# Kernel tuning notes

Hardware: AMD Instinct MI355X
Metric: run time of the kernel (lower is better)

## Reference

```python
import jax, jax.numpy as jnp
import numpy as np

NPG = 400          # nodes per graph (CC400 atlas ROIs)
B = 512            # graphs per batch
N = B * NPG        # total nodes
EPG = 6400         # edges per graph (avg degree 16)
E = B * EPG
F_IN = 200         # node feature dim
H = 64             # hidden_channels
C = 2              # num_classes


def _lin(k, fi, fo):
    return jax.random.normal(k, (fi, fo), jnp.float32) / np.sqrt(fi)


def setup_inputs() -> dict:
    key = jax.random.key(0)
    ks = jax.random.split(key, 16)
    # intra-graph edges: local src/dst in [0, NPG) plus per-graph offset
    g = jnp.repeat(jnp.arange(B, dtype=jnp.int32), EPG)
    src = jax.random.randint(ks[0], (E,), 0, NPG, dtype=jnp.int32) + g * NPG
    dst = jax.random.randint(ks[1], (E,), 0, NPG, dtype=jnp.int32) + g * NPG
    edge_index = jnp.stack([src, dst])  # [2, E]
    x = jax.random.normal(ks[2], (N, F_IN), jnp.float32)
    return dict(
        x=x, edge_index=edge_index, npg=NPG,
        # SAGEConv i: out = lin_l(mean_agg) + lin_r(x); lin_l carries the bias
        W1l=_lin(ks[3], F_IN, H), W1r=_lin(ks[4], F_IN, H), b1=jnp.zeros((H,), jnp.float32),
        W2l=_lin(ks[5], H, H), W2r=_lin(ks[6], H, H), b2=jnp.zeros((H,), jnp.float32),
        W3l=_lin(ks[7], H, H), W3r=_lin(ks[8], H, H), b3=jnp.zeros((H,), jnp.float32),
        # SAGPooling score GNN = GraphConv(H, 1): lin_rel(sum_agg) + lin_root(x)
        Wpr=_lin(ks[9], H, 1), bpr=jnp.zeros((1,), jnp.float32), Wpo=_lin(ks[10], H, 1),
        # final classifier
        Wlin=_lin(ks[11], H, C), blin=jnp.zeros((C,), jnp.float32),
    )


def reference(x, edge_index, npg, W1l, W1r, b1, W2l, W2r, b2, W3l, W3r, b3,
              Wpr, bpr, Wpo, Wlin, blin):
    n = x.shape[0]
    src, dst = edge_index[0], edge_index[1]

    deg = jax.ops.segment_sum(jnp.ones((src.shape[0],), x.dtype), dst, num_segments=n)
    inv_deg = 1.0 / jnp.maximum(deg, 1.0)  # [n]

    def sage(h, Wl, Wr, b):
        # mean aggregation over incoming edges, then lin_l(agg)+b + lin_r(h)
        agg = jax.ops.segment_sum(h[src], dst, num_segments=n) * inv_deg[:, None]
        return agg @ Wl + b + h @ Wr

    x1 = jax.nn.relu(sage(x, W1l, W1r, b1))
    x2 = jax.nn.relu(sage(x1, W2l, W2r, b2)) + x1
    x3 = jax.nn.relu(sage(x2, W3l, W3r, b3)) + x2

    # SAGPooling score via GraphConv (add aggregation)
    score = (jax.ops.segment_sum(x3[src], dst, num_segments=n) @ Wpr + bpr
             + x3 @ Wpo)[:, 0]  # [n]

    nb = n // npg            # number of graphs
    k = npg // 2             # ratio = 0.5, uniform graph sizes
    vals, idx = jax.lax.top_k(score.reshape(nb, npg), k)       # [nb, k]
    flat_idx = (jnp.arange(nb, dtype=idx.dtype)[:, None] * npg + idx).reshape(-1)
    xp = x3[flat_idx] * jnp.tanh(vals.reshape(-1))[:, None]    # [nb*k, H]

    pooled = xp.reshape(nb, k, -1).mean(axis=1)                # global_mean_pool
    logits = pooled @ Wlin + blin
    return jax.nn.log_softmax(logits, axis=1)
```

## Files before the change

kernel.cpp:

```cpp
#include <hip/hip_runtime.h>
#include <hip/hip_bf16.h>
#include <math.h>

#define F_IN 200
#define HDIM 64
#define NPG  400
#define EPG  6400
#define KSEL 200

typedef __attribute__((ext_vector_type(4))) float f32x4;
typedef __attribute__((ext_vector_type(8))) short s16x8;

__device__ __forceinline__ void gload_lds16(const void* g, void* l) {
    __builtin_amdgcn_global_load_lds(
        (const __attribute__((address_space(1))) void*)g,
        (__attribute__((address_space(3))) void*)l, 16, 0, 0);
}

__device__ __forceinline__ unsigned int bf16_rne(float x) {
    unsigned int b = __float_as_uint(x);
    return (b + 0x7FFFu + ((b >> 16) & 1u)) >> 16;
}

__device__ __forceinline__ void split8(f32x4 v0, f32x4 v1, s16x8& h, s16x8& l) {
    float x[8] = {v0.x, v0.y, v0.z, v0.w, v1.x, v1.y, v1.z, v1.w};
#pragma unroll
    for (int j = 0; j < 8; j++) {
        unsigned int hb = bf16_rne(x[j]);
        float hf = __uint_as_float(hb << 16);
        float r = x[j] - hf;
        unsigned int lb = bf16_rne(r);
        h[j] = (short)hb;
        l[j] = (short)lb;
    }
}

__global__ void pack_wf(const float* __restrict__ Wl, const float* __restrict__ Wr,
                        short* __restrict__ WF, int K, int KC) {
    int idx = blockIdx.x * blockDim.x + threadIdx.x;
    if (idx >= KC * 4096) return;
    int j    = idx & 7;
    int lane = (idx >> 3) & 63;
    int nf   = (idx >> 9) & 7;
    int kc   = idx >> 12;
    int k = kc * 32 + (lane >> 4) * 8 + j;
    int n = nf * 16 + (lane & 15);
    float v = 0.f;
    if (k < K) v = (n < 64) ? Wl[k * 64 + n] : Wr[k * 64 + (n - 64)];
    unsigned int hb = bf16_rne(v);
    float hf = __uint_as_float(hb << 16);
    unsigned int lb = bf16_rne(v - hf);
    WF[(size_t)((kc * 8 + nf) * 2 + 0) * 512 + lane * 8 + j] = (short)hb;
    WF[(size_t)((kc * 8 + nf) * 2 + 1) * 512 + lane * 8 + j] = (short)lb;
}

__global__ void pack_wf4(const float* __restrict__ Wl, const float* __restrict__ Wr,
                         short* __restrict__ WF) {
    int idx = blockIdx.x * blockDim.x + threadIdx.x;
    if (idx >= 4 * 2048) return;
    int j    = idx & 7;
    int lane = (idx >> 3) & 63;
    int nf   = (idx >> 9) & 3;
    int kc   = idx >> 11;
    int k = kc * 32 + (lane >> 4) * 8 + j;
    int n = nf * 16 + (lane & 15);
    float v = (k < 64) ? Wl[k * 64 + n] : Wr[(k - 64) * 64 + n];
    unsigned int hb = bf16_rne(v);
    float hf = __uint_as_float(hb << 16);
    unsigned int lb = bf16_rne(v - hf);
    WF[(size_t)((kc * 4 + nf) * 2 + 0) * 512 + lane * 8 + j] = (short)hb;
    WF[(size_t)((kc * 4 + nf) * 2 + 1) * 512 + lane * 8 + j] = (short)lb;
}

template <int K, int LDX, int KC, int TAIL>
__global__ __launch_bounds__(256) void gemm_lds(const float* __restrict__ X,
                                                const short* __restrict__ WF,
                                                float* __restrict__ O) {
    __shared__ float Xs[2][128 * 32];
    __shared__ short Ws[2][8 * 2 * 512];
    const int tid  = threadIdx.x;
    const int lane = tid & 63;
    const int wave = tid >> 6;
    const size_t rowbase = (size_t)blockIdx.x * 128;
    const f32x4 zero4 = (f32x4){0.f, 0.f, 0.f, 0.f};

    const int srow_off = wave * 32 + (lane >> 3);
    const int sbyte    = 16 * ((lane & 7) ^ (lane >> 3));

#define DMA_CHUNK(b, kc_) {                                                      \
    _Pragma("unroll")                                                            \
    for (int j = 0; j < 4; j++) {                                                \
        const char* xsrc = (const char*)X +                                      \
            (rowbase + srow_off + j * 8) * (size_t)(LDX * 4) + (kc_) * 128 + sbyte; \
        gload_lds16(xsrc, (char*)&Xs[b][0] + wave * 4096 + j * 1024);            \
        const short* wsrc = WF + (size_t)(kc_) * 8192 + wave * 2048 + j * 512 + lane * 8; \
        gload_lds16(wsrc, (char*)&Ws[b][0] + wave * 4096 + j * 1024);            \
    } }

    f32x4 acc[2][8];
#pragma unroll
    for (int m = 0; m < 2; m++)
#pragma unroll
        for (int nf = 0; nf < 8; nf++) acc[m][nf] = zero4;

    DMA_CHUNK(0, 0);
    __syncthreads();

    for (int kc = 0; kc < KC; kc++) {
        const int b = kc & 1;
        if (kc + 1 < KC) DMA_CHUNK(b ^ 1, kc + 1);

        s16x8 ah[2], al[2];
#pragma unroll
        for (int m = 0; m < 2; m++) {
            const int lr = wave * 32 + m * 16 + (lane & 15);
            const int g0 = (lane >> 4) * 2;
            f32x4 v0 = *(const f32x4*)&Xs[b][lr * 32 + 4 * (g0 ^ (lane & 7))];
            f32x4 v1 = *(const f32x4*)&Xs[b][lr * 32 + 4 * ((g0 + 1) ^ (lane & 7))];
            split8(v0, v1, ah[m], al[m]);
        }
#pragma unroll
        for (int nf = 0; nf < 8; nf++) {
            s16x8 wh = *(const s16x8*)&Ws[b][(nf * 2 + 0) * 512 + lane * 8];
            s16x8 wl = *(const s16x8*)&Ws[b][(nf * 2 + 1) * 512 + lane * 8];
#pragma unroll
            for (int m = 0; m < 2; m++) {
                acc[m][nf] = __builtin_amdgcn_mfma_f32_16x16x32_bf16(ah[m], wh, acc[m][nf], 0, 0, 0);
                acc[m][nf] = __builtin_amdgcn_mfma_f32_16x16x32_bf16(al[m], wh, acc[m][nf], 0, 0, 0);
                acc[m][nf] = __builtin_amdgcn_mfma_f32_16x16x32_bf16(ah[m], wl, acc[m][nf], 0, 0, 0);
            }
        }
        __syncthreads();
    }
#undef DMA_CHUNK

    if constexpr (TAIL > 0) {
        s16x8 ah[2], al[2];
#pragma unroll
        for (int m = 0; m < 2; m++) {
            const size_t row = rowbase + wave * 32 + m * 16 + (lane & 15);
            const int k0 = KC * 32 + (lane >> 4) * 8;
            f32x4 v0 = (k0 + 4 <= K) ? *(const f32x4*)&X[row * (size_t)LDX + k0] : zero4;
            f32x4 v1 = (k0 + 8 <= K) ? *(const f32x4*)&X[row * (size_t)LDX + k0 + 4] : zero4;
            split8(v0, v1, ah[m], al[m]);
        }
#pragma unroll
        for (int nf = 0; nf < 8; nf++) {
            s16x8 wh = *(const s16x8*)&WF[(size_t)((KC * 8 + nf) * 2 + 0) * 512 + lane * 8];
            s16x8 wl = *(const s16x8*)&WF[(size_t)((KC * 8 + nf) * 2 + 1) * 512 + lane * 8];
#pragma unroll
            for (int m = 0; m < 2; m++) {
                acc[m][nf] = __builtin_amdgcn_mfma_f32_16x16x32_bf16(ah[m], wh, acc[m][nf], 0, 0, 0);
                acc[m][nf] = __builtin_amdgcn_mfma_f32_16x16x32_bf16(al[m], wh, acc[m][nf], 0, 0, 0);
                acc[m][nf] = __builtin_amdgcn_mfma_f32_16x16x32_bf16(ah[m], wl, acc[m][nf], 0, 0, 0);
            }
        }
    }

    float* cs0 = &Xs[0][wave * 1024];
    float* cs1 = &Xs[1][wave * 1024];
#pragma unroll
    for (int m = 0; m < 2; m++) {
        const int scol = lane & 15;
        const int srow = (lane >> 4) * 4;
#pragma unroll
        for (int nf = 0; nf < 8; nf++)
#pragma unroll
            for (int r = 0; r < 4; r++) {
                int cr = srow + r;
                float* p = (cr < 8) ? cs0 + cr * 128 : cs1 + (cr - 8) * 128;
                p[nf * 16 + scol] = acc[m][nf][r];
            }
#pragma unroll
        for (int ps = 0; ps < 8; ps++) {
            int row = ps * 2 + (lane >> 5);
            const float* p = (row < 8) ? cs0 + row * 128 : cs1 + (row - 8) * 128;
            f32x4 v = *(const f32x4*)&p[(lane & 31) * 4];
            *(f32x4*)&O[(rowbase + wave * 32 + m * 16 + row) * 128 + (lane & 31) * 4] = v;
        }
    }
}

__global__ __launch_bounds__(256) void combine_ss(
    const float* __restrict__ M, const float* __restrict__ H,
    const short* __restrict__ WF, const float* __restrict__ bias,
    const float* __restrict__ resid, float* __restrict__ P)
{
    __shared__ float Xs[4][64 * 32];
    __shared__ short Ws[4][4096];
    const int tid  = threadIdx.x;
    const int lane = tid & 63;
    const int wave = tid >> 6;
    const size_t rowbase = (size_t)blockIdx.x * 64;

#pragma unroll
    for (int c = 0; c < 4; c++) {
        const float* srcbuf = (c < 2) ? M : H;
#pragma unroll
        for (int i = 0; i < 2; i++) {
            int rr = i * 8 + (lane >> 3);
            int jj = (lane & 7) ^ (rr & 7);
            const char* src = (const char*)(srcbuf + (rowbase + wave * 16 + rr) * 64)
                              + (c & 1) * 128 + jj * 16;
            gload_lds16(src, (char*)&Xs[c][0] + wave * 2048 + i * 1024 + lane * 16);
        }
#pragma unroll
        for (int t = 0; t < 2; t++) {
            int idx = t * 256 + tid;
            const short* wsrc = WF + (size_t)c * 4096 + idx * 8;
            gload_lds16(wsrc, (char*)&Ws[c][0] + idx * 16);
        }
    }
    __syncthreads();

    f32x4 acc[4];
#pragma unroll
    for (int nf = 0; nf < 4; nf++) acc[nf] = (f32x4){0.f, 0.f, 0.f, 0.f};

    const int r = lane & 15;
    const int j0 = (lane >> 4) * 2;
#pragma unroll
    for (int kc = 0; kc < 4; kc++) {
        const float* abase = &Xs[kc][wave * 512 + r * 32];
        f32x4 v0 = *(const f32x4*)&abase[((j0    ) ^ (r & 7)) * 4];
        f32x4 v1 = *(const f32x4*)&abase[((j0 + 1) ^ (r & 7)) * 4];
        s16x8 ah, al;
        split8(v0, v1, ah, al);
#pragma unroll
        for (int nf = 0; nf < 4; nf++) {
            s16x8 wh = *(const s16x8*)&Ws[kc][(nf * 2 + 0) * 512 + lane * 8];
            s16x8 wl = *(const s16x8*)&Ws[kc][(nf * 2 + 1) * 512 + lane * 8];
            acc[nf] = __builtin_amdgcn_mfma_f32_16x16x32_bf16(ah, wh, acc[nf], 0, 0, 0);
            acc[nf] = __builtin_amdgcn_mfma_f32_16x16x32_bf16(al, wh, acc[nf], 0, 0, 0);
            acc[nf] = __builtin_amdgcn_mfma_f32_16x16x32_bf16(ah, wl, acc[nf], 0, 0, 0);
        }
    }

    {
        float* cs0 = &Xs[0][wave * 512];
        float* cs1 = &Xs[1][wave * 512];
        const int scol = lane & 15;
        const int srow = (lane >> 4) * 4;
#pragma unroll
        for (int nf = 0; nf < 4; nf++)
#pragma unroll
            for (int ri = 0; ri < 4; ri++) {
                int cr = srow + ri;
                float* p = (cr < 8) ? cs0 + cr * 64 : cs1 + (cr - 8) * 64;
                p[nf * 16 + scol] = acc[nf][ri];
            }
#pragma unroll
        for (int i = 0; i < 4; i++) {
            int row = i * 4 + (lane >> 4);
            int col = (lane & 15) * 4;
            const float* p = (row < 8) ? cs0 + row * 64 : cs1 + (row - 8) * 64;
            f32x4 v = *(const f32x4*)&p[col];
            size_t grow = rowbase + wave * 16 + row;
            f32x4 bb = *(const f32x4*)&bias[col];
            f32x4 rr = *(const f32x4*)&resid[grow * 64 + col];
            f32x4 o;
#pragma unroll
            for (int q = 0; q < 4; q++) o[q] = fmaxf(v[q] + bb[q], 0.f) + rr[q];
            *(f32x4*)&P[grow * 64 + col] = o;
        }
    }
}

__global__ __launch_bounds__(256) void csr_build(
    const int* __restrict__ esrc, const int* __restrict__ edst,
    int* __restrict__ csr_src, int* __restrict__ rowptr,
    int* __restrict__ degs, float* __restrict__ invdeg)
{
    __shared__ int cnt[NPG];
    __shared__ int off[NPG];
    __shared__ int cur[NPG];
    const int g = blockIdx.x, tid = threadIdx.x;
    const int ebase = g * EPG, nodebase = g * NPG;
    for (int i = tid; i < NPG; i += 256) cnt[i] = 0;
    __syncthreads();
    for (int e = tid; e < EPG; e += 256)
        atomicAdd(&cnt[edst[ebase + e] - nodebase], 1);
    __syncthreads();
    if (tid == 0) {
        int run = 0;
        for (int i = 0; i < NPG; i++) { off[i] = run; run += cnt[i]; }
    }
    __syncthreads();
    for (int i = tid; i < NPG; i += 256) {
        cur[i] = off[i];
        rowptr[nodebase + i] = off[i];
        degs[nodebase + i] = cnt[i];
        invdeg[nodebase + i] = 1.f / fmaxf((float)cnt[i], 1.f);
    }
    __syncthreads();
    for (int e = tid; e < EPG; e += 256) {
        int ld = edst[ebase + e] - nodebase;
        int p = atomicAdd(&cur[ld], 1);
        csr_src[ebase + p] = esrc[ebase + e] - nodebase;
    }
}

__global__ __launch_bounds__(1024) void agg_lds(
    const float* __restrict__ A,
    const int* __restrict__ csr_src, const int* __restrict__ rowptr,
    const int* __restrict__ degs, const float* __restrict__ invdeg,
    const float* __restrict__ bias,
    float* __restrict__ Xout)
{
    __shared__ float y[NPG * 64];
    __shared__ int   csr_l[EPG];
    const int g = blockIdx.x, tid = threadIdx.x;
    const int ebase = g * EPG, nodebase = g * NPG;

    for (int idx = tid; idx < NPG * 16; idx += 1024) {
        int node = idx >> 4, c4 = (idx & 15) * 4;
        *(float4*)&y[node * 64 + c4] =
            *(const float4*)&A[(size_t)(nodebase + node) * 128 + c4];
    }
    for (int e = tid; e < EPG; e += 1024) csr_l[e] = csr_src[ebase + e];
    __syncthreads();

    const int wave = tid >> 6, lane = tid & 63;
    for (int node = wave; node < NPG; node += 16) {
        const int start = rowptr[nodebase + node];
        const int dg = degs[nodebase + node];
        float acc = 0.f;
        int j = 0;
        for (; j + 4 <= dg; j += 4) {
            int s0 = csr_l[start + j];
            int s1 = csr_l[start + j + 1];
            int s2 = csr_l[start + j + 2];
            int s3 = csr_l[start + j + 3];
            acc += y[s0 * 64 + lane] + y[s1 * 64 + lane]
                 + y[s2 * 64 + lane] + y[s3 * 64 + lane];
        }
        for (; j < dg; j++) acc += y[csr_l[start + j] * 64 + lane];

        float v = acc * invdeg[nodebase + node] + bias[lane]
                + A[(size_t)(nodebase + node) * 128 + 64 + lane];
        Xout[(size_t)(nodebase + node) * 64 + lane] = fmaxf(v, 0.f);
    }
}

__global__ __launch_bounds__(1024) void agg_in(
    const float* __restrict__ H,
    const int* __restrict__ csr_src, const int* __restrict__ rowptr,
    const int* __restrict__ degs, const float* __restrict__ invdeg,
    float* __restrict__ M)
{
    __shared__ float y[NPG * 64];
    __shared__ int   csr_l[EPG];
    const int g = blockIdx.x, tid = threadIdx.x;
    const int ebase = g * EPG, nodebase = g * NPG;

    for (int idx = tid; idx < NPG * 16; idx += 1024) {
        int node = idx >> 4, c4 = (idx & 15) * 4;
        *(float4*)&y[node * 64 + c4] =
            *(const float4*)&H[(size_t)(nodebase + node) * 64 + c4];
    }
    for (int e = tid; e < EPG; e += 1024) csr_l[e] = csr_src[ebase + e];
    __syncthreads();

    const int wave = tid >> 6, lane = tid & 63;
    for (int node = wave; node < NPG; node += 16) {
        const int start = rowptr[nodebase + node];
        const int dg = degs[nodebase + node];
        float acc = 0.f;
        int j = 0;
        for (; j + 4 <= dg; j += 4) {
            int s0 = csr_l[start + j];
            int s1 = csr_l[start + j + 1];
            int s2 = csr_l[start + j + 2];
            int s3 = csr_l[start + j + 3];
            acc += y[s0 * 64 + lane] + y[s1 * 64 + lane]
                 + y[s2 * 64 + lane] + y[s3 * 64 + lane];
        }
        for (; j < dg; j++) acc += y[csr_l[start + j] * 64 + lane];

        M[(size_t)(nodebase + node) * 64 + lane] = acc * invdeg[nodebase + node];
    }
}

__global__ __launch_bounds__(1024) void score_pool3(
    const float* __restrict__ X3,
    const int* __restrict__ esrc, const int* __restrict__ edst,
    const float* __restrict__ Wpr, const float* __restrict__ bpr,
    const float* __restrict__ Wpo,
    const float* __restrict__ Wlin, const float* __restrict__ blin,
    float* __restrict__ out)
{
    __shared__ float y[NPG * 64];
    __shared__ float t0s[NPG], ss[NPG], wsel[NPG];
    __shared__ float wprs[64], wpos[64];
    __shared__ float pp[16 * 64];
    __shared__ float pooled[64];
    __shared__ float lgs[2];
    const int g = blockIdx.x, tid = threadIdx.x;
    const int nodebase = g * NPG, ebase = g * EPG;

    if (tid < 64) { wprs[tid] = Wpr[tid]; wpos[tid] = Wpo[tid]; }
    for (int idx = tid; idx < NPG * 16; idx += 1024) {
        int node = idx >> 4, c4 = (idx & 15) * 4;
        *(float4*)&y[node * 64 + c4] =
            *(const float4*)&X3[(size_t)(nodebase + node) * 64 + c4];
    }
    __syncthreads();

    if (tid < NPG) {
        float a0 = 0.f, a1 = 0.f;
        const float* yr = &y[tid * 64];
#pragma unroll
        for (int i = 0; i < 64; i++) {
            int d = (tid + i) & 63;
            float v = yr[d];
            a0 += v * wprs[d];
            a1 += v * wpos[d];
        }
        t0s[tid] = a0;
        ss[tid] = bpr[0] + a1;
    }
    __syncthreads();
    for (int e = tid; e < EPG; e += 1024) {
        int ls = esrc[ebase + e] - nodebase;
        int ld = edst[ebase + e] - nodebase;
        atomicAdd(&ss[ld], t0s[ls]);
    }
    __syncthreads();
    if (tid < NPG) {
        float si = ss[tid];
        int cnt = 0;
        for (int j = 0; j < NPG; j++) {
            float sj = ss[j];
            cnt += (sj > si) || (sj == si && j < tid);
        }
        wsel[tid] = (cnt < KSEL) ? tanhf(si) * (1.f / KSEL) : 0.f;
    }
    __syncthreads();
    {
        const int d = tid & 63, part = tid >> 6;
        float a = 0.f;
        for (int i = part * 25; i < part * 25 + 25; i++)
            a += wsel[i] * y[i * 64 + d];
        pp[part * 64 + d] = a;
    }
    __syncthreads();
    if (tid < 64) {
        float s = 0.f;
#pragma unroll
        for (int i = 0; i < 16; i++) s += pp[i * 64 + tid];
        pooled[tid] = s;
    }
    __syncthreads();
    if (tid < 2) {
        float l = blin[tid];
        for (int d = 0; d < 64; d++) l += pooled[d] * Wlin[d * 2 + tid];
        lgs[tid] = l;
    }
    __syncthreads();
    if (tid < 2) {
        float m = fmaxf(lgs[0], lgs[1]);
        float lse = m + logf(expf(lgs[0] - m) + expf(lgs[1] - m));
        out[g * 2 + tid] = lgs[tid] - lse;
    }
}

extern "C" void kernel_launch(void* const* d_in, const int* in_sizes, int n_in,
                              void* d_out, int out_size, void* d_ws, size_t ws_size,
                              hipStream_t stream) {
    const float* x    = (const float*)d_in[0];
    const int*   eidx = (const int*)d_in[1];
    const float* W1l  = (const float*)d_in[3];
    const float* W1r  = (const float*)d_in[4];
    const float* b1   = (const float*)d_in[5];
    const float* W2l  = (const float*)d_in[6];
    const float* W2r  = (const float*)d_in[7];
    const float* b2   = (const float*)d_in[8];
    const float* W3l  = (const float*)d_in[9];
    const float* W3r  = (const float*)d_in[10];
    const float* b3   = (const float*)d_in[11];
    const float* Wpr  = (const float*)d_in[12];
    const float* bpr  = (const float*)d_in[13];
    const float* Wpo  = (const float*)d_in[14];
    const float* Wlin = (const float*)d_in[15];
    const float* blin = (const float*)d_in[16];

    const int N = in_sizes[0] / F_IN;
    const int E = in_sizes[1] / 2;
    const int B = N / NPG;
    const int* esrc = eidx;
    const int* edst = eidx + E;

    float* ws = (float*)d_ws;
    float* A      = ws;
    float* P0     = A + (size_t)N * 128;
    float* P1     = P0 + (size_t)N * 64;
    float* Mb     = P1 + (size_t)N * 64;
    float* invdeg = Mb + (size_t)N * 64;
    short* WF1    = (short*)(invdeg + N);
    short* WFc2   = WF1 + 57344;
    short* WFc3   = WFc2 + 16384;
    int*   csr    = (int*)(WFc3 + 16384);
    int*   rowptr = csr + E;
    int*   degs   = rowptr + N;

    pack_wf<<<(7 * 4096 + 255) / 256, 256, 0, stream>>>(W1l, W1r, WF1, 200, 7);
    pack_wf4<<<(4 * 2048 + 255) / 256, 256, 0, stream>>>(W2l, W2r, WFc2);
    pack_wf4<<<(4 * 2048 + 255) / 256, 256, 0, stream>>>(W3l, W3r, WFc3);

    csr_build<<<B, 256, 0, stream>>>(esrc, edst, csr, rowptr, degs, invdeg);

    gemm_lds<200, 200, 6, 8><<<N / 128, 256, 0, stream>>>(x, WF1, A);
    agg_lds<<<B, 1024, 0, stream>>>(A, csr, rowptr, degs, invdeg, b1, P0);

    agg_in<<<B, 1024, 0, stream>>>(P0, csr, rowptr, degs, invdeg, Mb);
    combine_ss<<<N / 64, 256, 0, stream>>>(Mb, P0, WFc2, b2, P0, P1);

    agg_in<<<B, 1024, 0, stream>>>(P1, csr, rowptr, degs, invdeg, Mb);
    combine_ss<<<N / 64, 256, 0, stream>>>(Mb, P1, WFc3, b3, P1, P0);

    score_pool3<<<B, 1024, 0, stream>>>(P0, esrc, edst,
                                        Wpr, bpr, Wpo, Wlin, blin,
                                        (float*)d_out);
}
```

Before: 438.2 us.

## Rewrite first-layer GEMM to stage full 64-row X tile in LDS

Replaces the double-buffered 128-row, 32-wide-chunk GEMM with a kernel that loads a whole 64x200 slab of X into padded LDS in one DMA pass. It then loops over K, reading the pre-split bf16 weight fragments straight from global memory (cached) rather than staging them in LDS. Rows per block drop from 128 to 64, which doubles the grid and halves the MFMA work per wave. The aim is fewer barriers and more occupancy and parallelism, at the cost of repeated global weight reads and no overlap between loading and compute.

```diff
diff --git a/kernel.cpp b/kernel.cpp
--- a/kernel.cpp
+++ b/kernel.cpp
@@ -72,111 +72,65 @@
     WF[(size_t)((kc * 4 + nf) * 2 + 1) * 512 + lane * 8 + j] = (short)lb;
 }
 
-template <int K, int LDX, int KC, int TAIL>
-__global__ __launch_bounds__(256) void gemm_lds(const float* __restrict__ X,
-                                                const short* __restrict__ WF,
-                                                float* __restrict__ O) {
-    __shared__ float Xs[2][128 * 32];
-    __shared__ short Ws[2][8 * 2 * 512];
-    const int tid  = threadIdx.x;
-    const int lane = tid & 63;
-    const int wave = tid >> 6;
-    const size_t rowbase = (size_t)blockIdx.x * 128;
+__global__ __launch_bounds__(256) void gemm1(const float* __restrict__ X,
+                                             const short* __restrict__ WF,
+                                             float* __restrict__ O) {
+    __shared__ float Xs[64 * 204];
+    const int tid = threadIdx.x, lane = tid & 63, wave = tid >> 6;
+    const size_t rowbase = (size_t)blockIdx.x * 64;
     const f32x4 zero4 = (f32x4){0.f, 0.f, 0.f, 0.f};
-
-    const int srow_off = wave * 32 + (lane >> 3);
-    const int sbyte    = 16 * ((lane & 7) ^ (lane >> 3));
-
-#define DMA_CHUNK(b, kc_) {                                                      \
-    _Pragma("unroll")                                                            \
-    for (int j = 0; j < 4; j++) {                                                \
-        const char* xsrc = (const char*)X +                                      \
-            (rowbase + srow_off + j * 8) * (size_t)(LDX * 4) + (kc_) * 128 + sbyte; \
-        gload_lds16(xsrc, (char*)&Xs[b][0] + wave * 4096 + j * 1024);            \
-        const short* wsrc = WF + (size_t)(kc_) * 8192 + wave * 2048 + j * 512 + lane * 8; \
-        gload_lds16(wsrc, (char*)&Ws[b][0] + wave * 4096 + j * 1024);            \
-    } }
-
-    f32x4 acc[2][8];
-#pragma unroll
-    for (int m = 0; m < 2; m++)
-#pragma unroll
-        for (int nf = 0; nf < 8; nf++) acc[m][nf] = zero4;
-
-    DMA_CHUNK(0, 0);
-    __syncthreads();
-
-    for (int kc = 0; kc < KC; kc++) {
-        const int b = kc & 1;
-        if (kc + 1 < KC) DMA_CHUNK(b ^ 1, kc + 1);
-
-        s16x8 ah[2], al[2];
-#pragma unroll
-        for (int m = 0; m < 2; m++) {
-            const int lr = wave * 32 + m * 16 + (lane & 15);
-            const int g0 = (lane >> 4) * 2;
-            f32x4 v0 = *(const f32x4*)&Xs[b][lr * 32 + 4 * (g0 ^ (lane & 7))];
-            f32x4 v1 = *(const f32x4*)&Xs[b][lr * 32 + 4 * ((g0 + 1) ^ (lane & 7))];
-            split8(v0, v1, ah[m], al[m]);
-        }
+    const s16x8* WFv = (const s16x8*)WF;
+
+#pragma unroll
+    for (int i = 0; i < 13; i++) {
+        int idx = i * 256 + tid;
+        if (idx < 64 * 51) {
+            int row = idx / 51, c16 = idx - row * 51;
+            int cc = (c16 < 50) ? c16 : 0;
+            const char* src = (const char*)X + (rowbase + row) * 800 + cc * 16;
+            gload_lds16(src, (char*)Xs + idx * 16);
+        }
+    }
+    __syncthreads();
+
+    f32x4 acc[8];
+#pragma unroll
+    for (int nf = 0; nf < 8; nf++) acc[nf] = zero4;
+
+    const int myrow = wave * 16 + (lane & 15);
+    const int kq = (lane >> 4) * 8;
+    for (int kc = 0; kc < 7; kc++) {
+        const int k0 = kc * 32 + kq;
+        f32x4 v0 = (k0 + 4 <= 200) ? *(const f32x4*)&Xs[myrow * 204 + k0] : zero4;
+        f32x4 v1 = (k0 + 8 <= 200) ? *(const f32x4*)&Xs[myrow * 204 + k0 + 4] : zero4;
+        s16x8 ah, al;
+        split8(v0, v1, ah, al);
+        const s16x8* wb = WFv + (size_t)(kc * 8) * 128 + lane;
 #pragma unroll
         for (int nf = 0; nf < 8; nf++) {
-            s16x8 wh = *(const s16x8*)&Ws[b][(nf * 2 + 0) * 512 + lane * 8];
-            s16x8 wl = *(const s16x8*)&Ws[b][(nf * 2 + 1) * 512 + lane * 8];
-#pragma unroll
-            for (int m = 0; m < 2; m++) {
-                acc[m][nf] = __builtin_amdgcn_mfma_f32_16x16x32_bf16(ah[m], wh, acc[m][nf], 0, 0, 0);
-                acc[m][nf] = __builtin_amdgcn_mfma_f32_16x16x32_bf16(al[m], wh, acc[m][nf], 0, 0, 0);
-                acc[m][nf] = __builtin_amdgcn_mfma_f32_16x16x32_bf16(ah[m], wl, acc[m][nf], 0, 0, 0);
-            }
-        }
-        __syncthreads();
-    }
-#undef DMA_CHUNK
-
-    if constexpr (TAIL > 0) {
-        s16x8 ah[2], al[2];
-#pragma unroll
-        for (int m = 0; m < 2; m++) {
-            const size_t row = rowbase + wave * 32 + m * 16 + (lane & 15);
-            const int k0 = KC * 32 + (lane >> 4) * 8;
-            f32x4 v0 = (k0 + 4 <= K) ? *(const f32x4*)&X[row * (size_t)LDX + k0] : zero4;
-            f32x4 v1 = (k0 + 8 <= K) ? *(const f32x4*)&X[row * (size_t)LDX + k0 + 4] : zero4;
-            split8(v0, v1, ah[m], al[m]);
-        }
-#pragma unroll
-        for (int nf = 0; nf < 8; nf++) {
-            s16x8 wh = *(const s16x8*)&WF[(size_t)((KC * 8 + nf) * 2 + 0) * 512 + lane * 8];
-            s16x8 wl = *(const s16x8*)&WF[(size_t)((KC * 8 + nf) * 2 + 1) * 512 + lane * 8];
-#pragma unroll
-            for (int m = 0; m < 2; m++) {
-                acc[m][nf] = __builtin_amdgcn_mfma_f32_16x16x32_bf16(ah[m], wh, acc[m][nf], 0, 0, 0);
-                acc[m][nf] = __builtin_amdgcn_mfma_f32_16x16x32_bf16(al[m], wh, acc[m][nf], 0, 0, 0);
-                acc[m][nf] = __builtin_amdgcn_mfma_f32_16x16x32_bf16(ah[m], wl, acc[m][nf], 0, 0, 0);
-            }
-        }
-    }
-
-    float* cs0 = &Xs[0][wave * 1024];
-    float* cs1 = &Xs[1][wave * 1024];
-#pragma unroll
-    for (int m = 0; m < 2; m++) {
+            s16x8 wh = wb[nf * 128];
+            s16x8 wl = wb[nf * 128 + 64];
+            acc[nf] = __builtin_amdgcn_mfma_f32_16x16x32_bf16(ah, wh, acc[nf], 0, 0, 0);
+            acc[nf] = __builtin_amdgcn_mfma_f32_16x16x32_bf16(al, wh, acc[nf], 0, 0, 0);
+            acc[nf] = __builtin_amdgcn_mfma_f32_16x16x32_bf16(ah, wl, acc[nf], 0, 0, 0);
+        }
+    }
+
+    {
+        float* cs = &Xs[wave * 3264];
         const int scol = lane & 15;
         const int srow = (lane >> 4) * 4;
 #pragma unroll
         for (int nf = 0; nf < 8; nf++)
 #pragma unroll
-            for (int r = 0; r < 4; r++) {
-                int cr = srow + r;
-                float* p = (cr < 8) ? cs0 + cr * 128 : cs1 + (cr - 8) * 128;
-                p[nf * 16 + scol] = acc[m][nf][r];
-            }
+            for (int ri = 0; ri < 4; ri++)
+                cs[(srow + ri) * 132 + nf * 16 + scol] = acc[nf][ri];
 #pragma unroll
         for (int ps = 0; ps < 8; ps++) {
             int row = ps * 2 + (lane >> 5);
-            const float* p = (row < 8) ? cs0 + row * 128 : cs1 + (row - 8) * 128;
-            f32x4 v = *(const f32x4*)&p[(lane & 31) * 4];
-            *(f32x4*)&O[(rowbase + wave * 32 + m * 16 + row) * 128 + (lane & 31) * 4] = v;
+            int col = (lane & 31) * 4;
+            f32x4 v = *(const f32x4*)&cs[row * 132 + col];
+            *(f32x4*)&O[(rowbase + wave * 16 + row) * 128 + col] = v;
         }
     }
 }
@@ -509,7 +463,7 @@
 
     csr_build<<<B, 256, 0, stream>>>(esrc, edst, csr, rowptr, degs, invdeg);
 
-    gemm_lds<200, 200, 6, 8><<<N / 128, 256, 0, stream>>>(x, WF1, A);
+    gemm1<<<N / 64, 256, 0, stream>>>(x, WF1, A);
     agg_lds<<<B, 1024, 0, stream>>>(A, csr, rowptr, degs, invdeg, b1, P0);
 
     agg_in<<<B, 1024, 0, stream>>>(P0, csr, rowptr, degs, invdeg, Mb);
```

After: 473.7 us. 8.1% more time.
